# Performance work log

Measured on AMD Instinct MI355X. Metric: run time of the kernel, lower is better.

Reference implementation:

```python
import jax, jax.numpy as jnp
import numpy as np

SEQ_LEN = 4096
INPUT_SIZE = 1024
OUTPUT_SIZE = 1024


def _xavier(key, shape):
    n = shape[0]
    lim = 1.0 / (n ** 0.5)
    return jax.random.uniform(key, shape, minval=-lim, maxval=lim, dtype=jnp.float32)


def setup_inputs() -> dict:
    key = jax.random.key(0)
    kx, kk, kv, kq = jax.random.split(key, 4)
    X = jax.random.normal(kx, (SEQ_LEN, INPUT_SIZE), dtype=jnp.float32)
    Wk = _xavier(kk, (INPUT_SIZE, OUTPUT_SIZE))
    Wv = _xavier(kv, (INPUT_SIZE, OUTPUT_SIZE))
    Wq = _xavier(kq, (INPUT_SIZE, OUTPUT_SIZE))
    return {"X": X, "Wk": Wk, "Wv": Wv, "Wq": Wq}


def reference(X, Wk, Wv, Wq):
    # Faithful to original: scores = K @ Q^T (note K first, no 1/sqrt(d) scaling)
    K = X @ Wk  # (S, D)
    V = X @ Wv  # (S, D)
    Q = X @ Wq  # (S, D)
    scores = jnp.einsum('sd,td->st', K, Q)  # (S, S) == K @ Q^T
    attn = jax.nn.softmax(scores, axis=-1) @ V  # (S, D)
    return attn
```

## Files before the change

kernel.cpp:

```cpp
#include <hip/hip_runtime.h>
#include <hip/hip_fp16.h>
#include <cstdint>

#define SEQ 4096
#define DIM 1024

typedef _Float16 f16x8 __attribute__((ext_vector_type(8)));
typedef float f32x16 __attribute__((ext_vector_type(16)));
typedef __attribute__((address_space(1))) void as1_void;
typedef __attribute__((address_space(3))) void as3_void;

__device__ __forceinline__ ushort f2h(float f) {
  _Float16 h = (_Float16)f;
  return __builtin_bit_cast(ushort, h);
}

__global__ void convert_all_kernel(const float* __restrict__ X, const float* __restrict__ Wk,
                                   const float* __restrict__ Wv, const float* __restrict__ Wq,
                                   ushort* __restrict__ Xh, ushort* __restrict__ Wt) {
  const int z = blockIdx.z;
  const int tx = threadIdx.x, ty = threadIdx.y;
  if (z == 3) {
    const int bid = blockIdx.y * 32 + blockIdx.x;
    const int t = ty * 32 + tx;
#pragma unroll
    for (int k = 0; k < 4; k++) {
      int i = bid * 1024 + k * 256 + t;
      float4 v = reinterpret_cast<const float4*>(X)[i];
      ushort4 o = { f2h(v.x), f2h(v.y), f2h(v.z), f2h(v.w) };
      reinterpret_cast<ushort4*>(Xh)[i] = o;
    }
    return;
  }
  __shared__ float tile[32][33];
  const float* W = (z == 0) ? Wk : (z == 1) ? Wv : Wq;
  int n0 = blockIdx.x * 32, k0 = blockIdx.y * 32;
#pragma unroll
  for (int r = 0; r < 4; r++) {
    int k = ty + r * 8;
    tile[k][tx] = W[(size_t)(k0 + k) * DIM + n0 + tx];
  }
  __syncthreads();
  ushort* out = Wt + (size_t)z * DIM * DIM;
#pragma unroll
  for (int r = 0; r < 4; r++) {
    int n = ty + r * 8;
    out[(size_t)(n0 + n) * DIM + k0 + tx] = f2h(tile[tx][n]);
  }
}

__device__ __forceinline__ void gemm_tile256(const ushort* __restrict__ A,
                                             const ushort* __restrict__ B,
                                             ushort* __restrict__ C,
                                             int N, int K, int m0, int n0,
                                             int kt0, int ktend) {
  constexpr int BK = 64;
  __shared__ __align__(16) ushort As[2][256 * BK];
  __shared__ __align__(16) ushort Bs[2][256 * BK];
  const int tid = threadIdx.x;
  const int wave = tid >> 6, lane = tid & 63;
  const int l31 = lane & 31, khalf = lane >> 5;
  const int wm = (wave & 1) * 128, wn = (wave >> 1) * 64;

  const int srow = tid >> 3;
  const int skey = ((srow & 7) ^ ((srow >> 3) & 3));
  const int sce = (((tid & 7) ^ skey) * 8);
  const int rk = (l31 & 7) ^ ((l31 >> 3) & 3);

  f32x16 acc[4][2];
#pragma unroll
  for (int i = 0; i < 4; i++)
#pragma unroll
    for (int j = 0; j < 2; j++)
#pragma unroll
      for (int r = 0; r < 16; r++) acc[i][j][r] = 0.f;

  const ushort* Abase = A + (size_t)(m0 + srow) * K + sce;
  const ushort* Bbase = B + (size_t)(n0 + srow) * K + sce;
  const int ldsbase = wave * 512;

  auto stage = [&](int buf, int kt) {
#pragma unroll
    for (int q = 0; q < 4; q++)
      __builtin_amdgcn_global_load_lds((const as1_void*)(Abase + (size_t)q * 64 * K + kt),
                                       (as3_void*)&As[buf][ldsbase + q * 4096], 16, 0, 0);
#pragma unroll
    for (int q = 0; q < 4; q++)
      __builtin_amdgcn_global_load_lds((const as1_void*)(Bbase + (size_t)q * 64 * K + kt),
                                       (as3_void*)&Bs[buf][ldsbase + q * 4096], 16, 0, 0);
  };

  const int ntiles = (ktend - kt0) >> 6;

  stage(0, kt0);
  stage(1, kt0 + BK);
  asm volatile("s_waitcnt vmcnt(8)" ::: "memory");
  __builtin_amdgcn_s_barrier();

  for (int tt = 0; tt < ntiles; ++tt) {
    const int cur = tt & 1;
    const ushort* As_c = As[cur];
    const ushort* Bs_c = Bs[cur];
#pragma unroll
    for (int ks = 0; ks < 4; ks++) {
      f16x8 af[4], bf2[2];
      const int co = (((ks * 2 + khalf) ^ rk) * 8);
#pragma unroll
      for (int i = 0; i < 4; i++)
        af[i] = *reinterpret_cast<const f16x8*>(&As_c[(wm + i * 32 + l31) * BK + co]);
#pragma unroll
      for (int j = 0; j < 2; j++)
        bf2[j] = *reinterpret_cast<const f16x8*>(&Bs_c[(wn + j * 32 + l31) * BK + co]);
      __builtin_amdgcn_s_barrier();
      __builtin_amdgcn_s_setprio(1);
#pragma unroll
      for (int i = 0; i < 4; i++)
#pragma unroll
        for (int j = 0; j < 2; j++)
          acc[i][j] = __builtin_amdgcn_mfma_f32_32x32x16_f16(af[i], bf2[j], acc[i][j], 0, 0, 0);
      __builtin_amdgcn_s_setprio(0);
    }
    __builtin_amdgcn_s_barrier();
    if (tt + 2 < ntiles) {
      stage(cur, kt0 + (tt + 2) * BK);
      asm volatile("s_waitcnt vmcnt(8)" ::: "memory");
      __builtin_amdgcn_s_barrier();
    } else if (tt + 1 < ntiles) {
      asm volatile("s_waitcnt vmcnt(0)" ::: "memory");
      __builtin_amdgcn_s_barrier();
    }
  }

#pragma unroll
  for (int i = 0; i < 4; i++)
#pragma unroll
    for (int j = 0; j < 2; j++)
#pragma unroll
      for (int r = 0; r < 16; r++) {
        int row = m0 + wm + i * 32 + (r & 3) + 8 * (r >> 2) + 4 * khalf;
        int col = n0 + wn + j * 32 + l31;
        C[(size_t)row * N + col] = f2h(acc[i][j][r]);
      }
}

__global__ __launch_bounds__(512, 2) void proj256_kernel(const ushort* __restrict__ Xh,
                                                         const ushort* __restrict__ Wt,
                                                         ushort* __restrict__ Kh,
                                                         ushort* __restrict__ Qh,
                                                         ushort* __restrict__ Vt) {
  const int b = blockIdx.x;
  const ushort* A;
  const ushort* B;
  ushort* Cp;
  int N, m0, n0;
  if (b < 128) {
    const int z = b >> 6, q = b & 63;
    A = Xh;
    B = Wt + (size_t)(z ? 2 : 0) * DIM * DIM;
    Cp = z ? Qh : Kh;
    N = DIM;
    m0 = (q >> 2) * 256;
    n0 = (q & 3) * 256;
  } else {
    const int q = b - 128;
    A = Wt + (size_t)DIM * DIM;
    B = Xh;
    Cp = Vt;
    N = SEQ;
    m0 = (q >> 4) * 256;
    n0 = (q & 15) * 256;
  }
  gemm_tile256(A, B, Cp, N, DIM, m0, n0, 0, DIM);
}

__global__ __launch_bounds__(512, 2) void score256_kernel(const ushort* __restrict__ Kh,
                                                          const ushort* __restrict__ Qh,
                                                          ushort* __restrict__ S) {
  const int f = blockIdx.x;
  const int t = (f & 7) * 32 + (f >> 3);
  gemm_tile256(Kh, Qh, S, SEQ, DIM, (t >> 4) * 256, (t & 15) * 256, 0, DIM);
}

__global__ __launch_bounds__(512, 2) void out256_kernel(const ushort* __restrict__ P,
                                                        const ushort* __restrict__ Vt,
                                                        ushort* __restrict__ Part) {
  const int f = blockIdx.x;
  const int z = f >> 6;
  const int q = f & 63;
  const int t = (q & 7) * 8 + (q >> 3);
  ushort* Cp = Part + (size_t)z * SEQ * DIM;
  gemm_tile256(P, Vt, Cp, DIM, SEQ, (t >> 2) * 256, (t & 3) * 256,
               z * (SEQ / 4), (z + 1) * (SEQ / 4));
}

__global__ void reduce4_kernel(const ushort* __restrict__ Part, float* __restrict__ out, int n8) {
  int i = blockIdx.x * blockDim.x + threadIdx.x;
  if (i >= n8) return;
  const f16x8* p0 = reinterpret_cast<const f16x8*>(Part);
  const f16x8* p1 = p0 + n8;
  const f16x8* p2 = p1 + n8;
  const f16x8* p3 = p2 + n8;
  f16x8 a = p0[i], b = p1[i], c = p2[i], d = p3[i];
  float4 lo, hi;
  lo.x = (float)a[0] + (float)b[0] + (float)c[0] + (float)d[0];
  lo.y = (float)a[1] + (float)b[1] + (float)c[1] + (float)d[1];
  lo.z = (float)a[2] + (float)b[2] + (float)c[2] + (float)d[2];
  lo.w = (float)a[3] + (float)b[3] + (float)c[3] + (float)d[3];
  hi.x = (float)a[4] + (float)b[4] + (float)c[4] + (float)d[4];
  hi.y = (float)a[5] + (float)b[5] + (float)c[5] + (float)d[5];
  hi.z = (float)a[6] + (float)b[6] + (float)c[6] + (float)d[6];
  hi.w = (float)a[7] + (float)b[7] + (float)c[7] + (float)d[7];
  reinterpret_cast<float4*>(out)[i * 2] = lo;
  reinterpret_cast<float4*>(out)[i * 2 + 1] = hi;
}

__global__ __launch_bounds__(256) void softmax_kernel(const ushort* __restrict__ S,
                                                      ushort* __restrict__ P) {
  const int wave = threadIdx.x >> 6, lane = threadIdx.x & 63;
  const int row = blockIdx.x * 4 + wave;
  const ushort* s = S + (size_t)row * SEQ;
  float v[64];
#pragma unroll
  for (int i = 0; i < 8; i++) {
    f16x8 h = reinterpret_cast<const f16x8*>(s)[i * 64 + lane];
#pragma unroll
    for (int j = 0; j < 8; j++) v[i * 8 + j] = (float)h[j];
  }
  float m = v[0];
#pragma unroll
  for (int j = 1; j < 64; j++) m = fmaxf(m, v[j]);
#pragma unroll
  for (int o = 32; o > 0; o >>= 1) m = fmaxf(m, __shfl_xor(m, o, 64));
  float sum = 0.f;
#pragma unroll
  for (int j = 0; j < 64; j++) {
    v[j] = __expf(v[j] - m);
    sum += v[j];
  }
#pragma unroll
  for (int o = 32; o > 0; o >>= 1) sum += __shfl_xor(sum, o, 64);
  float inv = 1.0f / sum;
  ushort* p = P + (size_t)row * SEQ;
#pragma unroll
  for (int i = 0; i < 8; i++) {
    f16x8 h;
#pragma unroll
    for (int j = 0; j < 8; j++) h[j] = (_Float16)(v[i * 8 + j] * inv);
    reinterpret_cast<f16x8*>(p)[i * 64 + lane] = h;
  }
}

extern "C" void kernel_launch(void* const* d_in, const int* in_sizes, int n_in,
                              void* d_out, int out_size, void* d_ws, size_t ws_size,
                              hipStream_t stream) {
  const float* X = (const float*)d_in[0];
  const float* Wk = (const float*)d_in[1];
  const float* Wv = (const float*)d_in[2];
  const float* Wq = (const float*)d_in[3];

  char* ws = (char*)d_ws;
  size_t off = 0;
  ushort* Xh = (ushort*)(ws + off); off += (size_t)SEQ * DIM * 2;
  ushort* Wt = (ushort*)(ws + off); off += (size_t)3 * DIM * DIM * 2;
  ushort* Kh = (ushort*)(ws + off); off += (size_t)SEQ * DIM * 2;
  ushort* Qh = (ushort*)(ws + off); off += (size_t)SEQ * DIM * 2;
  ushort* Vt = (ushort*)(ws + off); off += (size_t)SEQ * DIM * 2;
  ushort* S = (ushort*)(ws + off);  off += (size_t)SEQ * SEQ * 2;
  ushort* P = (ushort*)(ws + off);  off += (size_t)SEQ * SEQ * 2;

  ushort* Part = S;

  convert_all_kernel<<<dim3(32, 32, 4), dim3(32, 8), 0, stream>>>(X, Wk, Wv, Wq, Xh, Wt);
  proj256_kernel<<<256, 512, 0, stream>>>(Xh, Wt, Kh, Qh, Vt);
  score256_kernel<<<256, 512, 0, stream>>>(Kh, Qh, S);
  softmax_kernel<<<1024, 256, 0, stream>>>(S, P);
  out256_kernel<<<256, 512, 0, stream>>>(P, Vt, Part);
  reduce4_kernel<<<SEQ * DIM / 8 / 256, 256, 0, stream>>>(Part, (float*)d_out, SEQ * DIM / 8);
}
```

Measured before the change: 213.6 us.

## Interleave next-tile prefetch with MFMA steps using k-chunk-major LDS layout

Replaces the GEMM tile routine with a version that stores A/B tiles in LDS in k-chunk-major order (8 halves per row per chunk), which drops the XOR swizzle while keeping fragment reads contiguous. Loads for the next k-tile are split into four quarter-stages issued between the MFMA sub-steps of the current tile, with waitcnt and barrier points at ks=0 and ks=2. This aims to overlap global-to-LDS traffic with compute instead of staging everything at the tile boundary. The projection grid is also shrunk to 192 blocks, removing 64 V-projection blocks whose tiles fell outside the 1024-row output. The new global access pattern gives each consecutive thread a different row (16B each), which may coalesce worse, and the extra barriers per tile add sync cost.

After: 247.4 us. 15.8% more time.

```diff
diff --git a/kernel.cpp b/kernel.cpp
--- a/kernel.cpp
+++ b/kernel.cpp
@@ -49,23 +49,22 @@
   }
 }
 
-__device__ __forceinline__ void gemm_tile256(const ushort* __restrict__ A,
-                                             const ushort* __restrict__ B,
-                                             ushort* __restrict__ C,
-                                             int N, int K, int m0, int n0,
-                                             int kt0, int ktend) {
+__device__ __forceinline__ void gemm256p(const ushort* __restrict__ A,
+                                         const ushort* __restrict__ B,
+                                         ushort* __restrict__ C,
+                                         int N, int K, int m0, int n0,
+                                         int kt0, int ktend) {
   constexpr int BK = 64;
-  __shared__ __align__(16) ushort As[2][256 * BK];
-  __shared__ __align__(16) ushort Bs[2][256 * BK];
+  __shared__ __align__(16) ushort AsB[2][16384];
+  __shared__ __align__(16) ushort BsB[2][16384];
   const int tid = threadIdx.x;
   const int wave = tid >> 6, lane = tid & 63;
   const int l31 = lane & 31, khalf = lane >> 5;
   const int wm = (wave & 1) * 128, wn = (wave >> 1) * 64;
 
-  const int srow = tid >> 3;
-  const int skey = ((srow & 7) ^ ((srow >> 3) & 3));
-  const int sce = (((tid & 7) ^ skey) * 8);
-  const int rk = (l31 & 7) ^ ((l31 >> 3) & 3);
+  const int strow = tid & 255;
+  const int skc = tid >> 8;
+  const int sldsu = wave * 512;
 
   f32x16 acc[4][2];
 #pragma unroll
@@ -75,42 +74,62 @@
 #pragma unroll
       for (int r = 0; r < 16; r++) acc[i][j][r] = 0.f;
 
-  const ushort* Abase = A + (size_t)(m0 + srow) * K + sce;
-  const ushort* Bbase = B + (size_t)(n0 + srow) * K + sce;
-  const int ldsbase = wave * 512;
-
-  auto stage = [&](int buf, int kt) {
-#pragma unroll
-    for (int q = 0; q < 4; q++)
-      __builtin_amdgcn_global_load_lds((const as1_void*)(Abase + (size_t)q * 64 * K + kt),
-                                       (as3_void*)&As[buf][ldsbase + q * 4096], 16, 0, 0);
-#pragma unroll
-    for (int q = 0; q < 4; q++)
-      __builtin_amdgcn_global_load_lds((const as1_void*)(Bbase + (size_t)q * 64 * K + kt),
-                                       (as3_void*)&Bs[buf][ldsbase + q * 4096], 16, 0, 0);
+  const ushort* Asrc = A + (size_t)(m0 + strow) * K + skc * 8;
+  const ushort* Bsrc = B + (size_t)(n0 + strow) * K + skc * 8;
+  const int ntiles = (ktend - kt0) >> 6;
+
+  auto stageA = [&](int buf, int kt, int kh) {
+#pragma unroll
+    for (int q = 0; q < 2; q++)
+      __builtin_amdgcn_global_load_lds(
+          (const as1_void*)(Asrc + kt + kh * 32 + q * 16),
+          (as3_void*)&AsB[buf][kh * 8192 + q * 4096 + sldsu], 16, 0, 0);
   };
-
-  const int ntiles = (ktend - kt0) >> 6;
-
-  stage(0, kt0);
-  stage(1, kt0 + BK);
-  asm volatile("s_waitcnt vmcnt(8)" ::: "memory");
-  __builtin_amdgcn_s_barrier();
+  auto stageB = [&](int buf, int kt, int kh) {
+#pragma unroll
+    for (int q = 0; q < 2; q++)
+      __builtin_amdgcn_global_load_lds(
+          (const as1_void*)(Bsrc + kt + kh * 32 + q * 16),
+          (as3_void*)&BsB[buf][kh * 8192 + q * 4096 + sldsu], 16, 0, 0);
+  };
+
+  stageA(0, kt0, 0);
+  stageB(0, kt0, 0);
+  stageA(0, kt0, 1);
+  stageB(0, kt0, 1);
 
   for (int tt = 0; tt < ntiles; ++tt) {
-    const int cur = tt & 1;
-    const ushort* As_c = As[cur];
-    const ushort* Bs_c = Bs[cur];
+    const int cur = tt & 1, nb = cur ^ 1;
+    const int nkt = kt0 + (tt + 1) * BK;
+    const bool pf = (tt + 1 < ntiles);
+    const ushort* As_c = AsB[cur];
+    const ushort* Bs_c = BsB[cur];
 #pragma unroll
     for (int ks = 0; ks < 4; ks++) {
+      if (ks == 0) {
+        asm volatile("s_waitcnt vmcnt(4)" ::: "memory");
+        __builtin_amdgcn_s_barrier();
+      }
+      if (ks == 2) {
+        if (pf) asm volatile("s_waitcnt vmcnt(4)" ::: "memory");
+        else    asm volatile("s_waitcnt vmcnt(0)" ::: "memory");
+        __builtin_amdgcn_s_barrier();
+      }
+      const int ck = ks * 2 + khalf;
+      const int pb = (ck >> 2) * 8192 + (ck & 3) * 2048;
       f16x8 af[4], bf2[2];
-      const int co = (((ks * 2 + khalf) ^ rk) * 8);
 #pragma unroll
       for (int i = 0; i < 4; i++)
-        af[i] = *reinterpret_cast<const f16x8*>(&As_c[(wm + i * 32 + l31) * BK + co]);
+        af[i] = *reinterpret_cast<const f16x8*>(&As_c[pb + (wm + i * 32 + l31) * 8]);
 #pragma unroll
       for (int j = 0; j < 2; j++)
-        bf2[j] = *reinterpret_cast<const f16x8*>(&Bs_c[(wn + j * 32 + l31) * BK + co]);
+        bf2[j] = *reinterpret_cast<const f16x8*>(&Bs_c[pb + (wn + j * 32 + l31) * 8]);
+      if (pf) {
+        if (ks == 0) stageA(nb, nkt, 0);
+        if (ks == 1) stageB(nb, nkt, 0);
+        if (ks == 2) stageA(nb, nkt, 1);
+        if (ks == 3) stageB(nb, nkt, 1);
+      }
       __builtin_amdgcn_s_barrier();
       __builtin_amdgcn_s_setprio(1);
 #pragma unroll
@@ -119,15 +138,7 @@
         for (int j = 0; j < 2; j++)
           acc[i][j] = __builtin_amdgcn_mfma_f32_32x32x16_f16(af[i], bf2[j], acc[i][j], 0, 0, 0);
       __builtin_amdgcn_s_setprio(0);
-    }
-    __builtin_amdgcn_s_barrier();
-    if (tt + 2 < ntiles) {
-      stage(cur, kt0 + (tt + 2) * BK);
-      asm volatile("s_waitcnt vmcnt(8)" ::: "memory");
-      __builtin_amdgcn_s_barrier();
-    } else if (tt + 1 < ntiles) {
-      asm volatile("s_waitcnt vmcnt(0)" ::: "memory");
-      __builtin_amdgcn_s_barrier();
+      if (ks < 3) __builtin_amdgcn_s_barrier();
     }
   }
 
@@ -149,28 +160,17 @@
                                                          ushort* __restrict__ Qh,
                                                          ushort* __restrict__ Vt) {
   const int b = blockIdx.x;
-  const ushort* A;
-  const ushort* B;
-  ushort* Cp;
-  int N, m0, n0;
-  if (b < 128) {
-    const int z = b >> 6, q = b & 63;
-    A = Xh;
-    B = Wt + (size_t)(z ? 2 : 0) * DIM * DIM;
-    Cp = z ? Qh : Kh;
-    N = DIM;
-    m0 = (q >> 2) * 256;
-    n0 = (q & 3) * 256;
+  if (b < 64) {
+    gemm256p(Xh, Wt, Kh, DIM, DIM, (b >> 2) * 256, (b & 3) * 256, 0, DIM);
+  } else if (b < 128) {
+    const int q = b - 64;
+    gemm256p(Xh, Wt + (size_t)2 * DIM * DIM, Qh, DIM, DIM,
+             (q >> 2) * 256, (q & 3) * 256, 0, DIM);
   } else {
     const int q = b - 128;
-    A = Wt + (size_t)DIM * DIM;
-    B = Xh;
-    Cp = Vt;
-    N = SEQ;
-    m0 = (q >> 4) * 256;
-    n0 = (q & 15) * 256;
-  }
-  gemm_tile256(A, B, Cp, N, DIM, m0, n0, 0, DIM);
+    gemm256p(Wt + (size_t)DIM * DIM, Xh, Vt, SEQ, DIM,
+             (q >> 4) * 256, (q & 15) * 256, 0, DIM);
+  }
 }
 
 __global__ __launch_bounds__(512, 2) void score256_kernel(const ushort* __restrict__ Kh,
@@ -178,7 +178,7 @@
                                                           ushort* __restrict__ S) {
   const int f = blockIdx.x;
   const int t = (f & 7) * 32 + (f >> 3);
-  gemm_tile256(Kh, Qh, S, SEQ, DIM, (t >> 4) * 256, (t & 15) * 256, 0, DIM);
+  gemm256p(Kh, Qh, S, SEQ, DIM, (t >> 4) * 256, (t & 15) * 256, 0, DIM);
 }
 
 __global__ __launch_bounds__(512, 2) void out256_kernel(const ushort* __restrict__ P,
@@ -189,8 +189,8 @@
   const int q = f & 63;
   const int t = (q & 7) * 8 + (q >> 3);
   ushort* Cp = Part + (size_t)z * SEQ * DIM;
-  gemm_tile256(P, Vt, Cp, DIM, SEQ, (t >> 2) * 256, (t & 3) * 256,
-               z * (SEQ / 4), (z + 1) * (SEQ / 4));
+  gemm256p(P, Vt, Cp, DIM, SEQ, (t >> 2) * 256, (t & 3) * 256,
+           z * (SEQ / 4), (z + 1) * (SEQ / 4));
 }
 
 __global__ void reduce4_kernel(const ushort* __restrict__ Part, float* __restrict__ out, int n8) {
@@ -271,7 +271,7 @@
   ushort* Part = S;
 
   convert_all_kernel<<<dim3(32, 32, 4), dim3(32, 8), 0, stream>>>(X, Wk, Wv, Wq, Xh, Wt);
-  proj256_kernel<<<256, 512, 0, stream>>>(Xh, Wt, Kh, Qh, Vt);
+  proj256_kernel<<<192, 512, 0, stream>>>(Xh, Wt, Kh, Qh, Vt);
   score256_kernel<<<256, 512, 0, stream>>>(Kh, Qh, S);
   softmax_kernel<<<1024, 256, 0, stream>>>(S, P);
   out256_kernel<<<256, 512, 0, stream>>>(P, Vt, Part);
```
